# Kernel optimization log

Hardware: AMD Instinct MI355X
Metric: run time of the kernel (lower is better)

## Reference

```python
import jax, jax.numpy as jnp
import numpy as np

EMB = 512
HEADS = 8
HEAD_DIM = EMB // HEADS


def setup_inputs() -> dict:
    key = jax.random.key(0)
    ks = jax.random.split(key, 9)
    s = 1.0 / np.sqrt(EMB)
    return {
        "x": jax.random.normal(ks[0], (4, 2048, EMB), dtype=jnp.float32),
        "Wq": jax.random.uniform(ks[1], (EMB, EMB), jnp.float32, -s, s),
        "bq": jax.random.uniform(ks[2], (EMB,), jnp.float32, -s, s),
        "Wk": jax.random.uniform(ks[3], (EMB, EMB), jnp.float32, -s, s),
        "bk": jax.random.uniform(ks[4], (EMB,), jnp.float32, -s, s),
        "Wv": jax.random.uniform(ks[5], (EMB, EMB), jnp.float32, -s, s),
        "bv": jax.random.uniform(ks[6], (EMB,), jnp.float32, -s, s),
        "Wp": jax.random.uniform(ks[7], (EMB, EMB), jnp.float32, -s, s),
        "bp": jax.random.uniform(ks[8], (EMB,), jnp.float32, -s, s),
    }


def _split_heads(t):
    b, n, _ = t.shape
    return t.reshape(b, n, HEADS, HEAD_DIM).transpose(0, 2, 1, 3)  # b h n d


def reference(x, Wq, bq, Wk, bk, Wv, bv, Wp, bp):
    q = _split_heads(x @ Wq.T + bq)
    k = _split_heads(x @ Wk.T + bk)
    v = _split_heads(x @ Wv.T + bv)
    energy = jnp.einsum("bhqd,bhkd->bhqk", q, k)
    # NOTE: original applies softmax to UNSCALED logits, then divides probs by sqrt(emb)
    att = jax.nn.softmax(energy, axis=-1) / jnp.sqrt(jnp.float32(EMB))
    out = jnp.einsum("bhqk,bhkd->bhqd", att, v)
    b, h, n, d = out.shape
    out = out.transpose(0, 2, 1, 3).reshape(b, n, h * d)
    return out @ Wp.T + bp
```

## Files before the change

### kernel.cpp

```cpp
#include <hip/hip_runtime.h>
#include <math.h>
#include <stdint.h>

#define SEQ  2048
#define LOG2E 1.4426950408889634f

typedef __attribute__((ext_vector_type(4))) float f32x4;
typedef __attribute__((ext_vector_type(16))) float f32x16;
typedef __attribute__((ext_vector_type(8))) short bf16x8;

template <int V> struct IC { static constexpr int value = V; };

__device__ __forceinline__ unsigned packbf(float a, float b) {
    return __builtin_amdgcn_perm(__float_as_uint(b) + 0x8000u,
                                 __float_as_uint(a) + 0x8000u, 0x07060302u);
}

__global__ __launch_bounds__(256, 3) void qkv_kernel(
    const float* __restrict__ xf, const float* __restrict__ wqf,
    const float* __restrict__ wkf, const float* __restrict__ wvf,
    const float* __restrict__ bq, const float* __restrict__ bk,
    const float* __restrict__ bv,
    unsigned short* __restrict__ Qw, unsigned short* __restrict__ Kw,
    unsigned short* __restrict__ VTw)
{
    __shared__ __align__(16) unsigned short smem[8192];
    unsigned short* As = smem;
    unsigned short* Bs = smem + 4096;

    const int t = threadIdx.x;
    const int w = t >> 6, lane = t & 63, quad = (t >> 4) & 3, l15 = t & 15;
    const int wr = w >> 1, wc = w & 1;
    const int m0 = blockIdx.y * 128;
    const int n0 = blockIdx.x * 128;
    const int which = n0 >> 9;
    const float* wbase = which == 0 ? wqf : (which == 1 ? wkf : wvf);
    const int nrow = n0 & 511;

    const int ar = t >> 2, akq = t & 3;
    const float* ax = xf + (size_t)(m0 + ar) * 512 + akq * 8;
    const float* bx = wbase + (size_t)(nrow + ar) * 512 + akq * 8;
    const int lws = (ar & 15) | (akq << 4);
    const int off0 = (ar >> 4) * 512 + lws * 8;
    const int off1 = off0 + 4 * 512;

    f32x4 acc[4][4];
#pragma unroll
    for (int mt = 0; mt < 4; ++mt)
#pragma unroll
        for (int nt = 0; nt < 4; ++nt) acc[mt][nt] = (f32x4){0.f, 0.f, 0.f, 0.f};

    float4 ra[4], rb[4];
    auto loadt = [&](int k0) {
        ra[0] = *(const float4*)(ax + k0);
        ra[1] = *(const float4*)(ax + k0 + 4);
        ra[2] = *(const float4*)(ax + 32768 + k0);
        ra[3] = *(const float4*)(ax + 32768 + k0 + 4);
        rb[0] = *(const float4*)(bx + k0);
        rb[1] = *(const float4*)(bx + k0 + 4);
        rb[2] = *(const float4*)(bx + 32768 + k0);
        rb[3] = *(const float4*)(bx + 32768 + k0 + 4);
    };
    auto writet = [&]() {
        uint4 p;
        p.x = packbf(ra[0].x, ra[0].y); p.y = packbf(ra[0].z, ra[0].w);
        p.z = packbf(ra[1].x, ra[1].y); p.w = packbf(ra[1].z, ra[1].w);
        *(uint4*)(As + off0) = p;
        p.x = packbf(ra[2].x, ra[2].y); p.y = packbf(ra[2].z, ra[2].w);
        p.z = packbf(ra[3].x, ra[3].y); p.w = packbf(ra[3].z, ra[3].w);
        *(uint4*)(As + off1) = p;
        p.x = packbf(rb[0].x, rb[0].y); p.y = packbf(rb[0].z, rb[0].w);
        p.z = packbf(rb[1].x, rb[1].y); p.w = packbf(rb[1].z, rb[1].w);
        *(uint4*)(Bs + off0) = p;
        p.x = packbf(rb[2].x, rb[2].y); p.y = packbf(rb[2].z, rb[2].w);
        p.z = packbf(rb[3].x, rb[3].y); p.w = packbf(rb[3].z, rb[3].w);
        *(uint4*)(Bs + off1) = p;
    };

    loadt(0);
    auto kloop = [&](auto TRC) {
        constexpr int TR = decltype(TRC)::value;
        for (int ki = 0; ki < 16; ++ki) {
            writet();
            if (ki < 15) loadt((ki + 1) * 32);
            __syncthreads();
            bf16x8 af[4], bfr[4];
#pragma unroll
            for (int mt = 0; mt < 4; ++mt)
                af[mt] = *(const bf16x8*)(As + ((wr * 4 + mt) * 64 + lane) * 8);
#pragma unroll
            for (int nt = 0; nt < 4; ++nt)
                bfr[nt] = *(const bf16x8*)(Bs + ((wc * 4 + nt) * 64 + lane) * 8);
#pragma unroll
            for (int mt = 0; mt < 4; ++mt)
#pragma unroll
                for (int nt = 0; nt < 4; ++nt) {
                    if (TR)
                        acc[mt][nt] = __builtin_amdgcn_mfma_f32_16x16x32_bf16(
                            bfr[nt], af[mt], acc[mt][nt], 0, 0, 0);
                    else
                        acc[mt][nt] = __builtin_amdgcn_mfma_f32_16x16x32_bf16(
                            af[mt], bfr[nt], acc[mt][nt], 0, 0, 0);
                }
            if (ki < 15) __syncthreads();
        }
    };
    if (which < 2) kloop(IC<1>{});
    else           kloop(IC<0>{});

    if (which == 2) {
#pragma unroll
        for (int nt = 0; nt < 4; ++nt) {
            const int n = n0 + wc * 64 + nt * 16 + l15;
            const float bias = bv[n & 511];
            const int h = (n >> 6) & 7, d = n & 63;
#pragma unroll
            for (int mt = 0; mt < 4; ++mt) {
                const int mb = m0 + wr * 64 + mt * 16 + quad * 4;
                const int bi = mb >> 11, ns = mb & 2047;
                const int bhl = bi * 8 + h;
                const f32x4 v = acc[mt][nt];
                uint2 pk;
                pk.x = packbf(v[0] + bias, v[1] + bias);
                pk.y = packbf(v[2] + bias, v[3] + bias);
                const size_t off =
                    ((size_t)(bhl * 32 + (ns >> 6)) * 8 + ((d >> 5) << 2) +
                     ((ns >> 4) & 3)) * 512 +
                    ((d & 31) << 3) + ((ns & 8) << 5) + (ns & 7);
                *(uint2*)(VTw + off) = pk;
            }
        }
    } else {
        const float sc = which ? 1.f : LOG2E;
        const float* bpt = which ? bk : bq;
        unsigned short* base = which ? Kw : Qw;
#pragma unroll
        for (int nt = 0; nt < 4; ++nt) {
            const int nb = n0 + wc * 64 + nt * 16 + quad * 4;
            const f32x4 bvv = *(const f32x4*)(bpt + (nb & 511));
            const int h = (nb >> 6) & 7, d0 = nb & 63;
#pragma unroll
            for (int mt = 0; mt < 4; ++mt) {
                const int nsg = m0 + wr * 64 + mt * 16 + l15;
                const int bi = nsg >> 11, ns = nsg & 2047;
                const int bhl = bi * 8 + h;
                const f32x4 v = acc[mt][nt];
                uint2 pk;
                pk.x = packbf((v[0] + bvv[0]) * sc, (v[1] + bvv[1]) * sc);
                pk.y = packbf((v[2] + bvv[2]) * sc, (v[3] + bvv[3]) * sc);
                const size_t off =
                    ((size_t)(bhl * 64 + (ns >> 5)) * 4 + (d0 >> 4)) * 512 +
                    ((d0 & 8) << 5) + ((ns & 31) << 3) + (d0 & 7);
                *(uint2*)(base + off) = pk;
            }
        }
    }
}

__global__ __launch_bounds__(256, 3) void outproj_kernel(
    const unsigned short* __restrict__ Aw, const float* __restrict__ wpf,
    const float* __restrict__ bp, float* __restrict__ out)
{
    __shared__ __align__(16) unsigned short smem[6144];
    unsigned short* As = smem;
    unsigned short* Bs = smem + 4096;

    const int t = threadIdx.x;
    const int w = t >> 6, lane = t & 63, quad = (t >> 4) & 3, l15 = t & 15;
    const int wr = w >> 1, wc = w & 1;
    const int m0 = blockIdx.y * 128;
    const int n0 = blockIdx.x * 64;

    const int ar = t >> 2, akq = t & 3;
    const unsigned short* ap = Aw + (size_t)(m0 + ar) * 512 + akq * 8;
    const float* bx = wpf + (size_t)(n0 + ar) * 512 + akq * 8;
    const int lws = (ar & 15) | (akq << 4);
    const int off0 = (ar >> 4) * 512 + lws * 8;
    const int off1 = off0 + 4 * 512;
    const int boff = (ar >> 4) * 512 + lws * 8;

    f32x4 acc[4][2];
#pragma unroll
    for (int mt = 0; mt < 4; ++mt)
#pragma unroll
        for (int nt = 0; nt < 2; ++nt) acc[mt][nt] = (f32x4){0.f, 0.f, 0.f, 0.f};

    uint4 ra0, ra1;
    float4 rb0, rb1;
    auto loadt = [&](int k0) {
        ra0 = *(const uint4*)(ap + k0);
        ra1 = *(const uint4*)(ap + 32768 + k0);
        rb0 = *(const float4*)(bx + k0);
        rb1 = *(const float4*)(bx + k0 + 4);
    };
    auto writet = [&]() {
        *(uint4*)(As + off0) = ra0;
        *(uint4*)(As + off1) = ra1;
        uint4 p;
        p.x = packbf(rb0.x, rb0.y); p.y = packbf(rb0.z, rb0.w);
        p.z = packbf(rb1.x, rb1.y); p.w = packbf(rb1.z, rb1.w);
        *(uint4*)(Bs + boff) = p;
    };

    loadt(0);
    for (int ki = 0; ki < 16; ++ki) {
        writet();
        if (ki < 15) loadt((ki + 1) * 32);
        __syncthreads();
        bf16x8 af[4], bfr[2];
#pragma unroll
        for (int mt = 0; mt < 4; ++mt)
            af[mt] = *(const bf16x8*)(As + ((wr * 4 + mt) * 64 + lane) * 8);
#pragma unroll
        for (int nt = 0; nt < 2; ++nt)
            bfr[nt] = *(const bf16x8*)(Bs + ((wc * 2 + nt) * 64 + lane) * 8);
#pragma unroll
        for (int mt = 0; mt < 4; ++mt)
#pragma unroll
            for (int nt = 0; nt < 2; ++nt)
                acc[mt][nt] = __builtin_amdgcn_mfma_f32_16x16x32_bf16(
                    af[mt], bfr[nt], acc[mt][nt], 0, 0, 0);
        if (ki < 15) __syncthreads();
    }

#pragma unroll
    for (int nt = 0; nt < 2; ++nt) {
        const int n = n0 + wc * 32 + nt * 16 + l15;
        const float bias = bp[n];
#pragma unroll
        for (int mt = 0; mt < 4; ++mt) {
            const int mb = m0 + wr * 64 + mt * 16 + quad * 4;
            const f32x4 v = acc[mt][nt];
#pragma unroll
            for (int r = 0; r < 4; ++r)
                out[(size_t)(mb + r) * 512 + n] = v[r] + bias;
        }
    }
}

__global__ __launch_bounds__(512, 4) void attn_kernel(
    const unsigned short* __restrict__ Qf, const unsigned short* __restrict__ Kf,
    const unsigned short* __restrict__ Vf, unsigned short* __restrict__ Ow)
{
    __shared__ float cb[8448];
    const int t = threadIdx.x;
    const int w = t >> 6, lane = t & 63;
    const int l31 = lane & 31, hlf = lane >> 5;
    const int qi = w >> 1, jh = w & 1;

    const int bh = blockIdx.x;
    const int qblk = blockIdx.y;
    const int q0 = qblk * 128;

    const unsigned short* Kp = Kf + (size_t)bh * 131072 + (jh * 4) * 512 + lane * 8;
    const unsigned short* Vp = Vf + (size_t)bh * 131072 + lane * 8;

    const int qgg = qblk * 4 + qi;
    const unsigned short* Qp = Qf + ((size_t)(bh * 64 + qgg) * 4) * 512 + lane * 8;
    bf16x8 qf[4];
#pragma unroll
    for (int kt = 0; kt < 4; ++kt)
        qf[kt] = *(const bf16x8*)(Qp + kt * 512);

    f32x16 zero;
#pragma unroll
    for (int r = 0; r < 16; ++r) zero[r] = 0.f;

    float lpart = 0.f;
    f32x16 Ot[2];
    Ot[0] = zero; Ot[1] = zero;

    bf16x8 kc[4];
#pragma unroll
    for (int c = 0; c < 4; ++c)
        kc[c] = *(const bf16x8*)(Kp + c * 512);

    for (int jt = 0; jt < 32; ++jt) {
        bf16x8 vc[4];
#pragma unroll
        for (int dg = 0; dg < 2; ++dg)
#pragma unroll
            for (int p = 0; p < 2; ++p)
                vc[dg * 2 + p] = *(const bf16x8*)(
                    Vp + (size_t)jt * 4096 + (dg * 4 + jh * 2 + p) * 512);

        f32x16 st = zero;
        __builtin_amdgcn_s_setprio(1);
#pragma unroll
        for (int kt = 0; kt < 4; ++kt)
            st = __builtin_amdgcn_mfma_f32_32x32x16_bf16(kc[kt], qf[kt], st, 0, 0, 0);
        __builtin_amdgcn_s_setprio(0);

        const int jn = (jt < 31) ? jt + 1 : 31;
#pragma unroll
        for (int c = 0; c < 4; ++c)
            kc[c] = *(const bf16x8*)(Kp + (size_t)jn * 4096 + c * 512);

#pragma unroll
        for (int r = 0; r < 16; ++r)
            st[r] = __builtin_amdgcn_exp2f(st[r]);
        {
            float s01 = st[0] + st[1],   s23 = st[2] + st[3];
            float s45 = st[4] + st[5],   s67 = st[6] + st[7];
            float s89 = st[8] + st[9],   sAB = st[10] + st[11];
            float sCD = st[12] + st[13], sEF = st[14] + st[15];
            lpart += ((s01 + s23) + (s45 + s67)) + ((s89 + sAB) + (sCD + sEF));
        }

#pragma unroll
        for (int p = 0; p < 2; ++p) {
            const int r0 = p * 8;
            const unsigned a0 = packbf(st[r0 + 0], st[r0 + 1]);
            const unsigned a1 = packbf(st[r0 + 2], st[r0 + 3]);
            const unsigned b0 = packbf(st[r0 + 4], st[r0 + 5]);
            const unsigned b1 = packbf(st[r0 + 6], st[r0 + 7]);
            const unsigned ta0 = (unsigned)__shfl_xor((int)a0, 32);
            const unsigned ta1 = (unsigned)__shfl_xor((int)a1, 32);
            const unsigned tb0 = (unsigned)__shfl_xor((int)b0, 32);
            const unsigned tb1 = (unsigned)__shfl_xor((int)b1, 32);
            union { unsigned u[4]; bf16x8 v; } pb;
            pb.u[0] = hlf ? tb0 : a0;
            pb.u[1] = hlf ? tb1 : a1;
            pb.u[2] = hlf ? b0 : ta0;
            pb.u[3] = hlf ? b1 : ta1;
            __builtin_amdgcn_s_setprio(1);
            Ot[0] = __builtin_amdgcn_mfma_f32_32x32x16_bf16(vc[0 + p], pb.v, Ot[0], 0, 0, 0);
            Ot[1] = __builtin_amdgcn_mfma_f32_32x32x16_bf16(vc[2 + p], pb.v, Ot[1], 0, 0, 0);
            __builtin_amdgcn_s_setprio(0);
        }
    }

    if (jh == 1) {
#pragma unroll
        for (int dg = 0; dg < 2; ++dg) {
            const int cidx = (qi * 2 + dg) * 4;
#pragma unroll
            for (int k = 0; k < 4; ++k) {
                float4 v = make_float4(
                    Ot[dg][k * 4 + 0], Ot[dg][k * 4 + 1],
                    Ot[dg][k * 4 + 2], Ot[dg][k * 4 + 3]);
                *(float4*)(cb + (cidx + k) * 256 + lane * 4) = v;
            }
        }
        cb[8192 + qi * 64 + lane] = lpart;
    }
    __syncthreads();
    if (jh == 0) {
        const int bi = bh >> 3, h = bh & 7;
#pragma unroll
        for (int dg = 0; dg < 2; ++dg) {
            const int cidx = (qi * 2 + dg) * 4;
#pragma unroll
            for (int k = 0; k < 4; ++k) {
                const float4 v = *(const float4*)(cb + (cidx + k) * 256 + lane * 4);
                Ot[dg][k * 4 + 0] += v.x;
                Ot[dg][k * 4 + 1] += v.y;
                Ot[dg][k * 4 + 2] += v.z;
                Ot[dg][k * 4 + 3] += v.w;
            }
        }
        float lv = lpart + cb[8192 + qi * 64 + lane];
        lv += __shfl_xor(lv, 32);
        const float inv = 1.0f / (lv * 22.627416997969522f);

        const int ns = q0 + qi * 32 + l31;
        unsigned short* dst = Ow + ((size_t)bi * SEQ + ns) * 512 + h * 64 + hlf * 4;
#pragma unroll
        for (int dg = 0; dg < 2; ++dg)
#pragma unroll
            for (int rb2 = 0; rb2 < 4; ++rb2) {
                uint2 pk;
                pk.x = packbf(Ot[dg][rb2 * 4 + 0] * inv,
                              Ot[dg][rb2 * 4 + 1] * inv);
                pk.y = packbf(Ot[dg][rb2 * 4 + 2] * inv,
                              Ot[dg][rb2 * 4 + 3] * inv);
                *(uint2*)(dst + dg * 32 + rb2 * 8) = pk;
            }
    }
}

extern "C" void kernel_launch(void* const* d_in, const int* in_sizes, int n_in,
                              void* d_out, int out_size, void* d_ws, size_t ws_size,
                              hipStream_t stream)
{
    const float* x  = (const float*)d_in[0];
    const float* Wq = (const float*)d_in[1];
    const float* bq = (const float*)d_in[2];
    const float* Wk = (const float*)d_in[3];
    const float* bk = (const float*)d_in[4];
    const float* Wv = (const float*)d_in[5];
    const float* bv = (const float*)d_in[6];
    const float* Wp = (const float*)d_in[7];
    const float* bp = (const float*)d_in[8];

    unsigned short* ws = (unsigned short*)d_ws;
    unsigned short* Qw  = ws;
    unsigned short* Kw  = Qw + 4194304;
    unsigned short* VTw = Kw + 4194304;
    unsigned short* Owb = VTw + 4194304;

    qkv_kernel<<<dim3(12, 64), 256, 0, stream>>>(
        x, Wq, Wk, Wv, bq, bk, bv, Qw, Kw, VTw);
    attn_kernel<<<dim3(32, 16), 512, 0, stream>>>(Qw, Kw, VTw, Owb);
    outproj_kernel<<<dim3(8, 64), 256, 0, stream>>>(Owb, Wp, bp, (float*)d_out);
}
```

Before: 173.0 us.

## Software-pipeline QK^T MFMA one tile ahead of softmax and PV

The attention inner loop now computes the score tile for the next key block while running exp2, the row-sum and the PV MFMAs on the current tile, ping-ponging between two accumulators. K fragments are prefetched two tiles ahead. The aim is to overlap the dependent QK MFMA latency with the transcendental and shuffle work, at the cost of extra registers that could lower occupancy. The final iteration computes one redundant score tile that is never used.

```diff
diff --git a/kernel.cpp b/kernel.cpp
--- a/kernel.cpp
+++ b/kernel.cpp
@@ -275,7 +275,15 @@
     for (int c = 0; c < 4; ++c)
         kc[c] = *(const bf16x8*)(Kp + c * 512);
 
-    for (int jt = 0; jt < 32; ++jt) {
+    f32x16 stA = zero, stB = zero;
+#pragma unroll
+    for (int kt = 0; kt < 4; ++kt)
+        stA = __builtin_amdgcn_mfma_f32_32x32x16_bf16(kc[kt], qf[kt], stA, 0, 0, 0);
+#pragma unroll
+    for (int c = 0; c < 4; ++c)
+        kc[c] = *(const bf16x8*)(Kp + 4096 + c * 512);
+
+    auto step = [&](f32x16& stc, f32x16& stn, int jt) {
         bf16x8 vc[4];
 #pragma unroll
         for (int dg = 0; dg < 2; ++dg)
@@ -284,36 +292,36 @@
                 vc[dg * 2 + p] = *(const bf16x8*)(
                     Vp + (size_t)jt * 4096 + (dg * 4 + jh * 2 + p) * 512);
 
-        f32x16 st = zero;
+        stn = zero;
         __builtin_amdgcn_s_setprio(1);
 #pragma unroll
         for (int kt = 0; kt < 4; ++kt)
-            st = __builtin_amdgcn_mfma_f32_32x32x16_bf16(kc[kt], qf[kt], st, 0, 0, 0);
+            stn = __builtin_amdgcn_mfma_f32_32x32x16_bf16(kc[kt], qf[kt], stn, 0, 0, 0);
         __builtin_amdgcn_s_setprio(0);
 
-        const int jn = (jt < 31) ? jt + 1 : 31;
+        const int jn = (jt < 30) ? jt + 2 : 31;
 #pragma unroll
         for (int c = 0; c < 4; ++c)
             kc[c] = *(const bf16x8*)(Kp + (size_t)jn * 4096 + c * 512);
 
 #pragma unroll
         for (int r = 0; r < 16; ++r)
-            st[r] = __builtin_amdgcn_exp2f(st[r]);
+            stc[r] = __builtin_amdgcn_exp2f(stc[r]);
         {
-            float s01 = st[0] + st[1],   s23 = st[2] + st[3];
-            float s45 = st[4] + st[5],   s67 = st[6] + st[7];
-            float s89 = st[8] + st[9],   sAB = st[10] + st[11];
-            float sCD = st[12] + st[13], sEF = st[14] + st[15];
+            float s01 = stc[0] + stc[1],   s23 = stc[2] + stc[3];
+            float s45 = stc[4] + stc[5],   s67 = stc[6] + stc[7];
+            float s89 = stc[8] + stc[9],   sAB = stc[10] + stc[11];
+            float sCD = stc[12] + stc[13], sEF = stc[14] + stc[15];
             lpart += ((s01 + s23) + (s45 + s67)) + ((s89 + sAB) + (sCD + sEF));
         }
 
 #pragma unroll
         for (int p = 0; p < 2; ++p) {
             const int r0 = p * 8;
-            const unsigned a0 = packbf(st[r0 + 0], st[r0 + 1]);
-            const unsigned a1 = packbf(st[r0 + 2], st[r0 + 3]);
-            const unsigned b0 = packbf(st[r0 + 4], st[r0 + 5]);
-            const unsigned b1 = packbf(st[r0 + 6], st[r0 + 7]);
+            const unsigned a0 = packbf(stc[r0 + 0], stc[r0 + 1]);
+            const unsigned a1 = packbf(stc[r0 + 2], stc[r0 + 3]);
+            const unsigned b0 = packbf(stc[r0 + 4], stc[r0 + 5]);
+            const unsigned b1 = packbf(stc[r0 + 6], stc[r0 + 7]);
             const unsigned ta0 = (unsigned)__shfl_xor((int)a0, 32);
             const unsigned ta1 = (unsigned)__shfl_xor((int)a1, 32);
             const unsigned tb0 = (unsigned)__shfl_xor((int)b0, 32);
@@ -328,6 +336,11 @@
             Ot[1] = __builtin_amdgcn_mfma_f32_32x32x16_bf16(vc[2 + p], pb.v, Ot[1], 0, 0, 0);
             __builtin_amdgcn_s_setprio(0);
         }
+    };
+
+    for (int jt = 0; jt < 32; jt += 2) {
+        step(stA, stB, jt);
+        step(stB, stA, jt + 1);
     }
 
     if (jh == 1) {
```

Result: slower. 253.3 us (+46.4%).
